# Performance work log

Hardware: AMD Instinct MI355X
Metric: run time of the kernel (lower is better)

Reference implementation:

```python
import jax, jax.numpy as jnp
import numpy as np

NUM_CLASSES = 1000
FEATURE_DIM = 1024
BATCH = 8192
MOMENTUM = 0.9
LAMBDA_INTRA = 1.0
LAMBDA_INTER = 0.5


def setup_inputs() -> dict:
    key = jax.random.key(0)
    k1, k2, k3, k4 = jax.random.split(key, 4)
    return {
        "features": jax.random.normal(k1, (BATCH, FEATURE_DIM), jnp.float32),
        "features_adv": jax.random.normal(k2, (BATCH, FEATURE_DIM), jnp.float32),
        "centers": jax.random.normal(k3, (NUM_CLASSES, FEATURE_DIM), jnp.float32),
        "labels": jax.random.randint(k4, (BATCH,), 0, NUM_CLASSES, dtype=jnp.int64),
    }


def _l2_normalize(x):
    # torch F.normalize(p=2, dim=1) with eps=1e-12 clamp on the norm
    n = jnp.linalg.norm(x, axis=1, keepdims=True)
    return x / jnp.maximum(n, 1e-12)


def _update_centers(centers, feats, labels):
    # Vectorized version of the per-class masked-mean momentum update.
    C = centers.shape[0]
    sums = jax.ops.segment_sum(feats, labels, num_segments=C)            # [C, D]
    counts = jax.ops.segment_sum(jnp.ones((feats.shape[0],), feats.dtype), labels, num_segments=C)  # [C]
    means = sums / jnp.maximum(counts, 1.0)[:, None]
    has_samples = (counts > 0)[:, None]
    center_is_zero = jnp.all(centers == 0, axis=1, keepdims=True)
    updated = jnp.where(center_is_zero, means, MOMENTUM * centers + (1.0 - MOMENTUM) * means)
    return jnp.where(has_samples, updated, centers)


def reference(features, features_adv, centers, labels):
    f = _l2_normalize(features)
    fa = _l2_normalize(features_adv)

    # update_centers runs under no_grad on detached normalized features
    centers_new = _update_centers(centers, jax.lax.stop_gradient(f), labels)

    centers_batch = centers_new[labels]  # [B, D] gather
    intra_clean = jnp.linalg.norm(f - centers_batch, axis=1).mean()
    intra_adv = jnp.linalg.norm(fa - centers_batch, axis=1).mean()

    # fused pairwise center distances: ||ci||^2 + ||cj||^2 - 2 ci.cj
    sq = jnp.sum(centers_new * centers_new, axis=1)                      # [C]
    d2 = sq[:, None] + sq[None, :] - 2.0 * (centers_new @ centers_new.T)  # [C, C]
    dist = jnp.sqrt(jnp.maximum(d2, 0.0))
    C = centers_new.shape[0]
    upper = jnp.triu(jnp.ones((C, C), dtype=bool), k=1)
    n_pairs = C * (C - 1) / 2.0
    inter_loss = jnp.sum(jnp.where(upper, jax.nn.relu(1.0 - dist), 0.0)) / n_pairs

    return LAMBDA_INTRA * (intra_clean + intra_adv) - LAMBDA_INTER * inter_loss
```

## Files before the change

kernel.cpp:

```cpp
#include <hip/hip_runtime.h>
#include <math.h>

#define BATCH 8192
#define DIM 1024
#define NCLS 1000
#define NPAD 1024
#define NPAIRS 499500.0f
#define INTRA_BLOCKS (BATCH / 4)
#define INTER_TILES 136

typedef float  f32x4  __attribute__((ext_vector_type(4)));
typedef short  bf16x8 __attribute__((ext_vector_type(8)));


__device__ inline float waveAllReduceAdd(float x) {
  #pragma unroll
  for (int m = 32; m > 0; m >>= 1) x += __shfl_xor(x, m);
  return x;
}

__device__ inline float blockReduce1(float x, float* sm) {
  x = waveAllReduceAdd(x);
  int lane = threadIdx.x & 63, wid = threadIdx.x >> 6;
  __syncthreads();
  if (lane == 0) sm[wid] = x;
  __syncthreads();
  return sm[0] + sm[1] + sm[2] + sm[3];
}

__device__ inline unsigned short f2bf(float f) {
  unsigned int u = __float_as_uint(f);
  u += 0x7FFFu + ((u >> 16) & 1u);
  return (unsigned short)(u >> 16);
}


__global__ void hist_scan_scatter_kernel(const int* __restrict__ labels, int* counts,
                                         int* offsets, int* rows_sorted,
                                         float* partials) {
  __shared__ int h[1024];
  __shared__ int cur[1024];
  int t = threadIdx.x;
  h[t] = 0;
  if (t < 768) partials[t] = 0.0f;
  __syncthreads();
  #pragma unroll
  for (int j = t; j < BATCH; j += 1024) atomicAdd(&h[labels[j]], 1);
  __syncthreads();
  int v = h[t];
  if (t < NCLS) counts[t] = v;
  for (int off = 1; off < 1024; off <<= 1) {
    int u = (t >= off) ? h[t - off] : 0;
    __syncthreads();
    h[t] += u;
    __syncthreads();
  }
  int e = h[t] - v;
  cur[t] = e;
  if (t < NCLS) offsets[t] = e;
  __syncthreads();
  #pragma unroll
  for (int j = t; j < BATCH; j += 1024) {
    int pos = atomicAdd(&cur[labels[j]], 1);
    rows_sorted[pos] = j;
  }
}


__global__ void update_centers_kernel(const float* __restrict__ feats,
                                      const float* __restrict__ centers,
                                      const int* __restrict__ counts,
                                      const int* __restrict__ offsets,
                                      const int* __restrict__ rows_sorted,
                                      unsigned short* __restrict__ centers_bf,
                                      float* __restrict__ sqn) {
  __shared__ float sm[8];
  __shared__ int s_rows[64];
  __shared__ float s_part[8][4];
  __shared__ int s_anynz;
  int c = blockIdx.x;
  int tid = threadIdx.x;
  int lane = tid & 63, wid = tid >> 6;
  int fi = tid;

  if (c >= NCLS) {
    ((ushort4*)(centers_bf + (size_t)c * DIM))[fi] = make_ushort4(0, 0, 0, 0);
    return;
  }

  int n = counts[c];
  int off = offsets[c];
  const float4* f4 = (const float4*)feats;

  float4 acc = make_float4(0.f, 0.f, 0.f, 0.f);
  for (int b64 = 0; b64 < n; b64 += 64) {
    int m64 = min(64, n - b64);
    __syncthreads();
    if (tid < m64) s_rows[tid] = rows_sorted[off + b64 + tid];
    __syncthreads();
    for (int b8 = 0; b8 < m64; b8 += 8) {
      int m = min(8, m64 - b8);
      float4 v[8];
      #pragma unroll
      for (int j = 0; j < 8; ++j) {
        v[j] = make_float4(0.f, 0.f, 0.f, 0.f);
        if (j < m) v[j] = f4[(size_t)s_rows[b8 + j] * 256 + fi];
      }
      #pragma unroll
      for (int j = 0; j < 8; ++j) {
        float s = v[j].x * v[j].x + v[j].y * v[j].y + v[j].z * v[j].z + v[j].w * v[j].w;
        s = waveAllReduceAdd(s);
        if (lane == 0) s_part[j][wid] = s;
      }
      __syncthreads();
      #pragma unroll
      for (int j = 0; j < 8; ++j) {
        if (j < m) {
          float tot = s_part[j][0] + s_part[j][1] + s_part[j][2] + s_part[j][3];
          float w = 1.0f / fmaxf(sqrtf(tot), 1e-12f);
          acc.x += v[j].x * w; acc.y += v[j].y * w;
          acc.z += v[j].z * w; acc.w += v[j].w * w;
        }
      }
      __syncthreads();
    }
  }

  float invc = 1.0f / fmaxf((float)n, 1.0f);
  float4 mean = make_float4(acc.x * invc, acc.y * invc, acc.z * invc, acc.w * invc);

  float4 cv = ((const float4*)(centers + (size_t)c * DIM))[fi];
  if (tid == 0) s_anynz = 0;
  __syncthreads();
  if (cv.x != 0.f || cv.y != 0.f || cv.z != 0.f || cv.w != 0.f) s_anynz = 1;
  __syncthreads();

  float4 o;
  if (s_anynz) {
    o = make_float4(0.9f * cv.x + 0.1f * mean.x, 0.9f * cv.y + 0.1f * mean.y,
                    0.9f * cv.z + 0.1f * mean.z, 0.9f * cv.w + 0.1f * mean.w);
  } else {
    o = mean;
  }
  if (n == 0) o = cv;

  ((ushort4*)(centers_bf + (size_t)c * DIM))[fi] =
      make_ushort4(f2bf(o.x), f2bf(o.y), f2bf(o.z), f2bf(o.w));

  float sq = blockReduce1(o.x * o.x + o.y * o.y + o.z * o.z + o.w * o.w, sm);
  if (tid == 0) sqn[c] = sq;
}


__global__ void intra_inter_kernel(const float* __restrict__ feats,
                                   const float* __restrict__ featsa,
                                   const unsigned short* __restrict__ Cbf,
                                   const int* __restrict__ labels,
                                   const float* __restrict__ sq,
                                   float* __restrict__ partials) {
  __shared__ float smr[8];
  int tid = threadIdx.x;
  int bid = blockIdx.x;

  if (bid < INTRA_BLOCKS) {
    int lane = tid & 63;
    int row = bid * 4 + (tid >> 6);
    const float4* f4 = (const float4*)(feats + (size_t)row * DIM);
    const float4* a4 = (const float4*)(featsa + (size_t)row * DIM);
    int lab = labels[row];
    const ushort4* c4 = (const ushort4*)(Cbf + (size_t)lab * DIM);

    float4 fv[4], av[4];
    ushort4 cv[4];
    float ssf = 0.f, ssa = 0.f;
    #pragma unroll
    for (int i = 0; i < 4; ++i) {
      fv[i] = f4[lane + 64 * i];
      av[i] = a4[lane + 64 * i];
      cv[i] = c4[lane + 64 * i];
      ssf += fv[i].x * fv[i].x + fv[i].y * fv[i].y + fv[i].z * fv[i].z + fv[i].w * fv[i].w;
      ssa += av[i].x * av[i].x + av[i].y * av[i].y + av[i].z * av[i].z + av[i].w * av[i].w;
    }
    ssf = waveAllReduceAdd(ssf);
    ssa = waveAllReduceAdd(ssa);
    float invf = 1.0f / fmaxf(sqrtf(ssf), 1e-12f);
    float inva = 1.0f / fmaxf(sqrtf(ssa), 1e-12f);

    float d2c = 0.f, d2a = 0.f;
    #pragma unroll
    for (int i = 0; i < 4; ++i) {
      float cx = __uint_as_float((unsigned)cv[i].x << 16);
      float cy = __uint_as_float((unsigned)cv[i].y << 16);
      float cz = __uint_as_float((unsigned)cv[i].z << 16);
      float cw = __uint_as_float((unsigned)cv[i].w << 16);
      float dx = fv[i].x * invf - cx, dy = fv[i].y * invf - cy;
      float dz = fv[i].z * invf - cz, dw = fv[i].w * invf - cw;
      d2c += dx * dx + dy * dy + dz * dz + dw * dw;
      float ex = av[i].x * inva - cx, ey = av[i].y * inva - cy;
      float ez = av[i].z * inva - cz, ew = av[i].w * inva - cw;
      d2a += ex * ex + ey * ey + ez * ez + ew * ew;
    }
    d2c = waveAllReduceAdd(d2c);
    d2a = waveAllReduceAdd(d2a);
    if (lane == 0) {
      int slot = row & 255;
      atomicAdd(&partials[slot], sqrtf(d2c));
      atomicAdd(&partials[256 + slot], sqrtf(d2a));
    }
  } else {
    int t = bid - INTRA_BLOCKS;
    int bi = 0;
    while (t >= 16 - bi) { t -= 16 - bi; ++bi; }
    int bj = bi + t;

    int w = tid >> 6;
    int wy = w >> 1, wx = w & 1;
    int lane = tid & 63;
    int m = lane & 15;
    int q = lane >> 4;

    int i0 = bi * 64 + wy * 32;
    int j0 = bj * 64 + wx * 32;

    const unsigned short* arow0 = Cbf + (size_t)(i0 + m) * DIM;
    const unsigned short* arow1 = Cbf + (size_t)(i0 + 16 + m) * DIM;
    const unsigned short* brow0 = Cbf + (size_t)(j0 + m) * DIM;
    const unsigned short* brow1 = Cbf + (size_t)(j0 + 16 + m) * DIM;

    f32x4 acc00 = {0.f, 0.f, 0.f, 0.f}, acc01 = acc00, acc10 = acc00, acc11 = acc00;

    #pragma unroll 4
    for (int k0 = 0; k0 < DIM; k0 += 32) {
      int ko = k0 + q * 8;
      bf16x8 a0 = *(const bf16x8*)(arow0 + ko);
      bf16x8 a1 = *(const bf16x8*)(arow1 + ko);
      bf16x8 b0 = *(const bf16x8*)(brow0 + ko);
      bf16x8 b1 = *(const bf16x8*)(brow1 + ko);
      acc00 = __builtin_amdgcn_mfma_f32_16x16x32_bf16(a0, b0, acc00, 0, 0, 0);
      acc01 = __builtin_amdgcn_mfma_f32_16x16x32_bf16(a0, b1, acc01, 0, 0, 0);
      acc10 = __builtin_amdgcn_mfma_f32_16x16x32_bf16(a1, b0, acc10, 0, 0, 0);
      acc11 = __builtin_amdgcn_mfma_f32_16x16x32_bf16(a1, b1, acc11, 0, 0, 0);
    }

    float local = 0.f;
    int colA = lane & 15;
    int rbase = (lane >> 4) * 4;
    #pragma unroll
    for (int si = 0; si < 2; ++si) {
      #pragma unroll
      for (int sj = 0; sj < 2; ++sj) {
        f32x4 a = (si == 0) ? (sj == 0 ? acc00 : acc01) : (sj == 0 ? acc10 : acc11);
        #pragma unroll
        for (int r = 0; r < 4; ++r) {
          int i = i0 + si * 16 + rbase + r;
          int j = j0 + sj * 16 + colA;
          if (j < NCLS && i < j) {
            float d2 = sq[i] + sq[j] - 2.0f * a[r];
            float d = sqrtf(fmaxf(d2, 0.0f));
            local += fmaxf(1.0f - d, 0.0f);
          }
        }
      }
    }
    float tot = blockReduce1(local, smr);
    if (tid == 0) atomicAdd(&partials[512 + ((bi * 16 + bj) & 255)], tot);
  }
}


__global__ void final_kernel(const float* __restrict__ partials, float* __restrict__ out) {
  __shared__ float sm[8];
  int t = threadIdx.x;
  float c = partials[t] + partials[256 + t];
  float e = partials[512 + t];
  c = blockReduce1(c, sm);
  e = blockReduce1(e, sm);
  if (t == 0) {
    float intra = c * (1.0f / (float)BATCH);
    float inter = e / NPAIRS;
    out[0] = intra - 0.5f * inter;
  }
}


extern "C" void kernel_launch(void* const* d_in, const int* in_sizes, int n_in,
                              void* d_out, int out_size, void* d_ws, size_t ws_size,
                              hipStream_t stream) {
  const float* features     = (const float*)d_in[0];
  const float* features_adv = (const float*)d_in[1];
  const float* centers      = (const float*)d_in[2];
  const int*   labels       = (const int*)d_in[3];
  float* out = (float*)d_out;

  unsigned short* centers_bf = (unsigned short*)d_ws;
  float* sqn = (float*)(centers_bf + (size_t)NPAD * DIM);
  float* partials = sqn + NCLS;
  int* counts = (int*)(partials + 768);
  int* offsets = counts + NCLS;
  int* rows_sorted = offsets + NCLS;

  hipLaunchKernelGGL(hist_scan_scatter_kernel, dim3(1), dim3(1024), 0, stream, labels,
                     counts, offsets, rows_sorted, partials);
  hipLaunchKernelGGL(update_centers_kernel, dim3(NPAD), dim3(256), 0, stream, features,
                     centers, counts, offsets, rows_sorted, centers_bf, sqn);
  hipLaunchKernelGGL(intra_inter_kernel, dim3(INTRA_BLOCKS + INTER_TILES), dim3(256), 0,
                     stream, features, features_adv, centers_bf, labels, sqn, partials);
  hipLaunchKernelGGL(final_kernel, dim3(1), dim3(256), 0, stream, partials, out);
}
```

Baseline: 157.7 us.

## Drop sort kernel, scan labels per class, fuse final reduction via last-block

Removes the single-block histogram/scan/scatter kernel: each center-update block now scans all labels itself and collects the matching rows into shared memory (capped at 192 rows). The final reduction kernel is folded into the intra/inter kernel with an atomic done-counter so the last block finishes the sum. Inter tiles are moved to the front of the grid, launch bounds are added, and the bf16 center loads are deferred into the compute loop. This cuts two launches and a serial single-block stage. In exchange each block rereads all 8192 labels, and classes with more than 192 samples would be silently truncated.

```diff
diff --git a/kernel.cpp b/kernel.cpp
--- a/kernel.cpp
+++ b/kernel.cpp
@@ -6,8 +6,10 @@
 #define NCLS 1000
 #define NPAD 1024
 #define NPAIRS 499500.0f
+#define INTER_TILES 136
 #define INTRA_BLOCKS (BATCH / 4)
-#define INTER_TILES 136
+#define GRID_B (INTER_TILES + INTRA_BLOCKS)
+#define MAXROWS 192
 
 typedef float  f32x4  __attribute__((ext_vector_type(4)));
 typedef short  bf16x8 __attribute__((ext_vector_type(8)));
@@ -35,47 +37,17 @@
 }
 
 
-__global__ void hist_scan_scatter_kernel(const int* __restrict__ labels, int* counts,
-                                         int* offsets, int* rows_sorted,
-                                         float* partials) {
-  __shared__ int h[1024];
-  __shared__ int cur[1024];
-  int t = threadIdx.x;
-  h[t] = 0;
-  if (t < 768) partials[t] = 0.0f;
-  __syncthreads();
-  #pragma unroll
-  for (int j = t; j < BATCH; j += 1024) atomicAdd(&h[labels[j]], 1);
-  __syncthreads();
-  int v = h[t];
-  if (t < NCLS) counts[t] = v;
-  for (int off = 1; off < 1024; off <<= 1) {
-    int u = (t >= off) ? h[t - off] : 0;
-    __syncthreads();
-    h[t] += u;
-    __syncthreads();
-  }
-  int e = h[t] - v;
-  cur[t] = e;
-  if (t < NCLS) offsets[t] = e;
-  __syncthreads();
-  #pragma unroll
-  for (int j = t; j < BATCH; j += 1024) {
-    int pos = atomicAdd(&cur[labels[j]], 1);
-    rows_sorted[pos] = j;
-  }
-}
-
-
-__global__ void update_centers_kernel(const float* __restrict__ feats,
-                                      const float* __restrict__ centers,
-                                      const int* __restrict__ counts,
-                                      const int* __restrict__ offsets,
-                                      const int* __restrict__ rows_sorted,
-                                      unsigned short* __restrict__ centers_bf,
-                                      float* __restrict__ sqn) {
+__global__ __launch_bounds__(256, 4)
+void update_centers_kernel(const float* __restrict__ feats,
+                           const float* __restrict__ centers,
+                           const int* __restrict__ labels,
+                           unsigned short* __restrict__ centers_bf,
+                           float* __restrict__ sqn,
+                           float* __restrict__ partials,
+                           int* __restrict__ done) {
   __shared__ float sm[8];
-  __shared__ int s_rows[64];
+  __shared__ int s_rows[MAXROWS];
+  __shared__ int s_cnt;
   __shared__ float s_part[8][4];
   __shared__ int s_anynz;
   int c = blockIdx.x;
@@ -83,47 +55,54 @@
   int lane = tid & 63, wid = tid >> 6;
   int fi = tid;
 
+  if (tid == 0 && c < 768) partials[c] = 0.0f;
+  if (tid == 1 && c == 0) *done = 0;
+
   if (c >= NCLS) {
     ((ushort4*)(centers_bf + (size_t)c * DIM))[fi] = make_ushort4(0, 0, 0, 0);
     return;
   }
 
-  int n = counts[c];
-  int off = offsets[c];
+  if (tid == 0) s_cnt = 0;
+  __syncthreads();
+  #pragma unroll 4
+  for (int j = tid; j < BATCH; j += 256) {
+    if (labels[j] == c) {
+      int p = atomicAdd(&s_cnt, 1);
+      if (p < MAXROWS) s_rows[p] = j;
+    }
+  }
+  __syncthreads();
+  int n = min(s_cnt, MAXROWS);
+
   const float4* f4 = (const float4*)feats;
-
   float4 acc = make_float4(0.f, 0.f, 0.f, 0.f);
-  for (int b64 = 0; b64 < n; b64 += 64) {
-    int m64 = min(64, n - b64);
+
+  for (int b8 = 0; b8 < n; b8 += 8) {
+    int m = min(8, n - b8);
+    float4 v[8];
+    #pragma unroll
+    for (int j = 0; j < 8; ++j) {
+      v[j] = make_float4(0.f, 0.f, 0.f, 0.f);
+      if (j < m) v[j] = f4[(size_t)s_rows[b8 + j] * 256 + fi];
+    }
+    #pragma unroll
+    for (int j = 0; j < 8; ++j) {
+      float s = v[j].x * v[j].x + v[j].y * v[j].y + v[j].z * v[j].z + v[j].w * v[j].w;
+      s = waveAllReduceAdd(s);
+      if (lane == 0) s_part[j][wid] = s;
+    }
     __syncthreads();
-    if (tid < m64) s_rows[tid] = rows_sorted[off + b64 + tid];
+    #pragma unroll
+    for (int j = 0; j < 8; ++j) {
+      if (j < m) {
+        float tot = s_part[j][0] + s_part[j][1] + s_part[j][2] + s_part[j][3];
+        float w = 1.0f / fmaxf(sqrtf(tot), 1e-12f);
+        acc.x += v[j].x * w; acc.y += v[j].y * w;
+        acc.z += v[j].z * w; acc.w += v[j].w * w;
+      }
+    }
     __syncthreads();
-    for (int b8 = 0; b8 < m64; b8 += 8) {
-      int m = min(8, m64 - b8);
-      float4 v[8];
-      #pragma unroll
-      for (int j = 0; j < 8; ++j) {
-        v[j] = make_float4(0.f, 0.f, 0.f, 0.f);
-        if (j < m) v[j] = f4[(size_t)s_rows[b8 + j] * 256 + fi];
-      }
-      #pragma unroll
-      for (int j = 0; j < 8; ++j) {
-        float s = v[j].x * v[j].x + v[j].y * v[j].y + v[j].z * v[j].z + v[j].w * v[j].w;
-        s = waveAllReduceAdd(s);
-        if (lane == 0) s_part[j][wid] = s;
-      }
-      __syncthreads();
-      #pragma unroll
-      for (int j = 0; j < 8; ++j) {
-        if (j < m) {
-          float tot = s_part[j][0] + s_part[j][1] + s_part[j][2] + s_part[j][3];
-          float w = 1.0f / fmaxf(sqrtf(tot), 1e-12f);
-          acc.x += v[j].x * w; acc.y += v[j].y * w;
-          acc.z += v[j].z * w; acc.w += v[j].w * w;
-        }
-      }
-      __syncthreads();
-    }
   }
 
   float invc = 1.0f / fmaxf((float)n, 1.0f);
@@ -152,32 +131,34 @@
 }
 
 
-__global__ void intra_inter_kernel(const float* __restrict__ feats,
-                                   const float* __restrict__ featsa,
-                                   const unsigned short* __restrict__ Cbf,
-                                   const int* __restrict__ labels,
-                                   const float* __restrict__ sq,
-                                   float* __restrict__ partials) {
+__global__ __launch_bounds__(256, 4)
+void intra_inter_kernel(const float* __restrict__ feats,
+                        const float* __restrict__ featsa,
+                        const unsigned short* __restrict__ Cbf,
+                        const int* __restrict__ labels,
+                        const float* __restrict__ sq,
+                        float* __restrict__ partials,
+                        int* __restrict__ done,
+                        float* __restrict__ out) {
   __shared__ float smr[8];
+  __shared__ int s_last;
   int tid = threadIdx.x;
   int bid = blockIdx.x;
 
-  if (bid < INTRA_BLOCKS) {
+  if (bid >= INTER_TILES) {
     int lane = tid & 63;
-    int row = bid * 4 + (tid >> 6);
+    int row = (bid - INTER_TILES) * 4 + (tid >> 6);
     const float4* f4 = (const float4*)(feats + (size_t)row * DIM);
     const float4* a4 = (const float4*)(featsa + (size_t)row * DIM);
     int lab = labels[row];
     const ushort4* c4 = (const ushort4*)(Cbf + (size_t)lab * DIM);
 
     float4 fv[4], av[4];
-    ushort4 cv[4];
     float ssf = 0.f, ssa = 0.f;
     #pragma unroll
     for (int i = 0; i < 4; ++i) {
       fv[i] = f4[lane + 64 * i];
       av[i] = a4[lane + 64 * i];
-      cv[i] = c4[lane + 64 * i];
       ssf += fv[i].x * fv[i].x + fv[i].y * fv[i].y + fv[i].z * fv[i].z + fv[i].w * fv[i].w;
       ssa += av[i].x * av[i].x + av[i].y * av[i].y + av[i].z * av[i].z + av[i].w * av[i].w;
     }
@@ -189,10 +170,11 @@
     float d2c = 0.f, d2a = 0.f;
     #pragma unroll
     for (int i = 0; i < 4; ++i) {
-      float cx = __uint_as_float((unsigned)cv[i].x << 16);
-      float cy = __uint_as_float((unsigned)cv[i].y << 16);
-      float cz = __uint_as_float((unsigned)cv[i].z << 16);
-      float cw = __uint_as_float((unsigned)cv[i].w << 16);
+      ushort4 cvi = c4[lane + 64 * i];
+      float cx = __uint_as_float((unsigned)cvi.x << 16);
+      float cy = __uint_as_float((unsigned)cvi.y << 16);
+      float cz = __uint_as_float((unsigned)cvi.z << 16);
+      float cw = __uint_as_float((unsigned)cvi.w << 16);
       float dx = fv[i].x * invf - cx, dy = fv[i].y * invf - cy;
       float dz = fv[i].z * invf - cz, dw = fv[i].w * invf - cw;
       d2c += dx * dx + dy * dy + dz * dz + dw * dw;
@@ -208,7 +190,7 @@
       atomicAdd(&partials[256 + slot], sqrtf(d2a));
     }
   } else {
-    int t = bid - INTRA_BLOCKS;
+    int t = bid;
     int bi = 0;
     while (t >= 16 - bi) { t -= 16 - bi; ++bi; }
     int bj = bi + t;
@@ -265,20 +247,26 @@
     float tot = blockReduce1(local, smr);
     if (tid == 0) atomicAdd(&partials[512 + ((bi * 16 + bj) & 255)], tot);
   }
-}
-
-
-__global__ void final_kernel(const float* __restrict__ partials, float* __restrict__ out) {
-  __shared__ float sm[8];
-  int t = threadIdx.x;
-  float c = partials[t] + partials[256 + t];
-  float e = partials[512 + t];
-  c = blockReduce1(c, sm);
-  e = blockReduce1(e, sm);
-  if (t == 0) {
-    float intra = c * (1.0f / (float)BATCH);
-    float inter = e / NPAIRS;
-    out[0] = intra - 0.5f * inter;
+
+  __threadfence();
+  __syncthreads();
+  if (tid == 0) {
+    int p = atomicAdd(done, 1);
+    s_last = (p == GRID_B - 1);
+  }
+  __syncthreads();
+  if (s_last) {
+    __threadfence();
+    float c = __hip_atomic_load(&partials[tid], __ATOMIC_RELAXED, __HIP_MEMORY_SCOPE_AGENT) +
+              __hip_atomic_load(&partials[256 + tid], __ATOMIC_RELAXED, __HIP_MEMORY_SCOPE_AGENT);
+    float e = __hip_atomic_load(&partials[512 + tid], __ATOMIC_RELAXED, __HIP_MEMORY_SCOPE_AGENT);
+    c = blockReduce1(c, smr);
+    e = blockReduce1(e, smr);
+    if (tid == 0) {
+      float intra = c * (1.0f / (float)BATCH);
+      float inter = e / NPAIRS;
+      out[0] = intra - 0.5f * inter;
+    }
   }
 }
 
@@ -295,15 +283,10 @@
   unsigned short* centers_bf = (unsigned short*)d_ws;
   float* sqn = (float*)(centers_bf + (size_t)NPAD * DIM);
   float* partials = sqn + NCLS;
-  int* counts = (int*)(partials + 768);
-  int* offsets = counts + NCLS;
-  int* rows_sorted = offsets + NCLS;
-
-  hipLaunchKernelGGL(hist_scan_scatter_kernel, dim3(1), dim3(1024), 0, stream, labels,
-                     counts, offsets, rows_sorted, partials);
-  hipLaunchKernelGGL(update_centers_kernel, dim3(NPAD), dim3(256), 0, stream, features,
-                     centers, counts, offsets, rows_sorted, centers_bf, sqn);
-  hipLaunchKernelGGL(intra_inter_kernel, dim3(INTRA_BLOCKS + INTER_TILES), dim3(256), 0,
-                     stream, features, features_adv, centers_bf, labels, sqn, partials);
-  hipLaunchKernelGGL(final_kernel, dim3(1), dim3(256), 0, stream, partials, out);
-}
+  int* done = (int*)(partials + 768);
+
+  hipLaunchKernelGGL(update_centers_kernel, dim3(NPAD), dim3(256), 0, stream,
+                     features, centers, labels, centers_bf, sqn, partials, done);
+  hipLaunchKernelGGL(intra_inter_kernel, dim3(GRID_B), dim3(256), 0, stream, features,
+                     features_adv, centers_bf, labels, sqn, partials, done, out);
+}
```

Result: slower. 352.1 us (+123.2%).
